# Optimization experiments

Hardware: AMD Instinct MI355X
Metric: run time of the kernel (lower is better)

Reference implementation:

```python
import jax, jax.numpy as jnp
import numpy as np

N_NODES = 100000
N_EDGES = 1600000
IN_C, HID_C, OUT_C = 128, 128, 64
BN_EPS = 1e-5


def _sage_conv(x, src, dst, w_self, w_neigh, b):
    # mean aggregation over incoming edges (gather -> segment-sum -> scale)
    deg = jax.ops.segment_sum(jnp.ones((src.shape[0],), x.dtype), dst, num_segments=N_NODES)
    agg = jax.ops.segment_sum(x[src], dst, num_segments=N_NODES)
    agg = agg / jnp.maximum(deg, 1.0)[:, None]
    return x @ w_self + agg @ w_neigh + b


def _batch_norm(x, gamma, beta):
    mean = x.mean(axis=0)
    var = x.var(axis=0)
    return (x - mean) * jax.lax.rsqrt(var + BN_EPS) * gamma + beta


def setup_inputs() -> dict:
    key = jax.random.key(0)
    ks = jax.random.split(key, 16)
    x = jax.random.normal(ks[0], (N_NODES, IN_C), dtype=jnp.float32)
    edge_index = jax.random.randint(ks[1], (2, N_EDGES), 0, N_NODES, dtype=jnp.int64)
    s = 0.05
    return {
        "x": x,
        "edge_index": edge_index,
        "w0_self": jax.random.normal(ks[2], (IN_C, HID_C), jnp.float32) * s,
        "w0_neigh": jax.random.normal(ks[3], (IN_C, HID_C), jnp.float32) * s,
        "b0": jnp.zeros((HID_C,), jnp.float32),
        "g0": jnp.ones((HID_C,), jnp.float32),
        "be0": jnp.zeros((HID_C,), jnp.float32),
        "w1_self": jax.random.normal(ks[4], (HID_C, HID_C), jnp.float32) * s,
        "w1_neigh": jax.random.normal(ks[5], (HID_C, HID_C), jnp.float32) * s,
        "b1": jnp.zeros((HID_C,), jnp.float32),
        "g1": jnp.ones((HID_C,), jnp.float32),
        "be1": jnp.zeros((HID_C,), jnp.float32),
        "w2_self": jax.random.normal(ks[6], (HID_C, OUT_C), jnp.float32) * s,
        "w2_neigh": jax.random.normal(ks[7], (HID_C, OUT_C), jnp.float32) * s,
        "b2": jnp.zeros((OUT_C,), jnp.float32),
    }


def reference(x, edge_index, w0_self, w0_neigh, b0, g0, be0,
              w1_self, w1_neigh, b1, g1, be1, w2_self, w2_neigh, b2):
    src, dst = edge_index[0], edge_index[1]
    # layer 0: conv -> BN -> ReLU (dropout is identity in eval)
    h = _sage_conv(x, src, dst, w0_self, w0_neigh, b0)
    h = jax.nn.relu(_batch_norm(h, g0, be0))
    # layer 1
    h = _sage_conv(h, src, dst, w1_self, w1_neigh, b1)
    h = jax.nn.relu(_batch_norm(h, g1, be1))
    # final conv + log_softmax
    h = _sage_conv(h, src, dst, w2_self, w2_neigh, b2)
    return jax.nn.log_softmax(h, axis=-1)
```

## Files before the change

kernel.cpp:

```cpp
#include <hip/hip_runtime.h>

typedef unsigned int uint;
typedef __attribute__((ext_vector_type(8))) short short8;
typedef __attribute__((ext_vector_type(4))) float f32x4;

#define N_NODES 100000
#define N_EDGES 1600000
#define NB_SCAN 391
#define CONVG_N 1563
#define EB 6250
#define TFG 12500

__device__ __forceinline__ float bflo(uint v) { return __uint_as_float(v << 16); }
__device__ __forceinline__ float bfhi(uint v) { return __uint_as_float(v & 0xffff0000u); }
__device__ __forceinline__ uint packbf2(float a, float b) {
    uint ua = __float_as_uint(a), ub = __float_as_uint(b);
    ua += 0x7fffu + ((ua >> 16) & 1u);
    ub += 0x7fffu + ((ub >> 16) & 1u);
    return (ua >> 16) | (ub & 0xffff0000u);
}

__device__ __forceinline__ void pack_w_body(const float* __restrict__ Wself,
                                            const float* __restrict__ Wneigh,
                                            uint* __restrict__ Wb, int OUTC, int NT, int i) {
    if (i >= 8 * NT * 64 * 4) return;
    int u = i & 3;
    int l = (i >> 2) & 63;
    int t = i >> 8;
    int c = t % NT, s = t / NT;
    int k = s * 32 + (l >> 4) * 8 + u * 2;
    int col = c * 16 + (l & 15);
    const float* W0 = (k < 128) ? (Wself + (size_t)k * OUTC)
                                : (Wneigh + (size_t)(k - 128) * OUTC);
    const float* W1 = (k + 1 < 128) ? (Wself + (size_t)(k + 1) * OUTC)
                                    : (Wneigh + (size_t)(k + 1 - 128) * OUTC);
    Wb[i] = packbf2(W0[col], W1[col]);
}

__global__ void prep_fused(const int* __restrict__ dst,
                           int* __restrict__ deg, int* __restrict__ rank,
                           const float* __restrict__ x, uint* __restrict__ ht2,
                           const float* __restrict__ w0s, const float* __restrict__ w0n, uint* __restrict__ wb0,
                           const float* __restrict__ w1s, const float* __restrict__ w1n, uint* __restrict__ wb1,
                           const float* __restrict__ w2s, const float* __restrict__ w2n, uint* __restrict__ wb2) {
    int b = blockIdx.x;
    int tid = threadIdx.x;
    if (b < EB) {
        int e = b * 256 + tid;
        if (e < N_EDGES) rank[e] = atomicAdd(&deg[dst[e]], 1);
    } else if (b < EB + TFG) {
        int i = (b - EB) * 256 + tid;
        if (i < N_NODES * 32) {
            int row = i >> 5, q = i & 31;
            float4 v = *(const float4*)(x + (size_t)row * 128 + q * 4);
            uint2 o;
            o.x = packbf2(v.x, v.y);
            o.y = packbf2(v.z, v.w);
            *(uint2*)(ht2 + (size_t)row * 64 + q * 2) = o;
        }
    } else if (b < EB + TFG + 64) {
        pack_w_body(w0s, w0n, wb0, 128, 8, (b - EB - TFG) * 256 + tid);
    } else if (b < EB + TFG + 128) {
        pack_w_body(w1s, w1n, wb1, 128, 8, (b - EB - TFG - 64) * 256 + tid);
    } else {
        pack_w_body(w2s, w2n, wb2, 64, 4, (b - EB - TFG - 128) * 256 + tid);
    }
}

__global__ void scan_blocksum(const int* __restrict__ deg, int* __restrict__ blk) {
    __shared__ int s[256];
    int i = blockIdx.x * 256 + threadIdx.x;
    s[threadIdx.x] = (i < N_NODES) ? deg[i] : 0;
    __syncthreads();
    for (int off = 128; off > 0; off >>= 1) {
        if (threadIdx.x < off) s[threadIdx.x] += s[threadIdx.x + off];
        __syncthreads();
    }
    if (threadIdx.x == 0) blk[blockIdx.x] = s[0];
}

__global__ void scan_blockoff(int* __restrict__ blk, int* __restrict__ row_ptr_last) {
    __shared__ int s[512];
    int t = threadIdx.x;
    int v = (t < NB_SCAN) ? blk[t] : 0;
    s[t] = v;
    __syncthreads();
    for (int off = 1; off < 512; off <<= 1) {
        int xv = (t >= off) ? s[t - off] : 0;
        __syncthreads();
        s[t] += xv;
        __syncthreads();
    }
    if (t < NB_SCAN) blk[t] = s[t] - v;
    if (t == NB_SCAN - 1) *row_ptr_last = s[t];
}

__global__ void scan_final(const int* __restrict__ deg, const int* __restrict__ blk,
                           int* __restrict__ row_ptr, float* __restrict__ invd) {
    __shared__ int s[256];
    int i = blockIdx.x * 256 + threadIdx.x;
    int v = (i < N_NODES) ? deg[i] : 0;
    s[threadIdx.x] = v;
    __syncthreads();
    for (int off = 1; off < 256; off <<= 1) {
        int xv = (threadIdx.x >= off) ? s[threadIdx.x - off] : 0;
        __syncthreads();
        s[threadIdx.x] += xv;
        __syncthreads();
    }
    if (i < N_NODES) {
        row_ptr[i] = blk[blockIdx.x] + s[threadIdx.x] - v;
        invd[i] = 1.0f / fmaxf((float)v, 1.0f);
    }
}

__global__ void fill_csr2(const int* __restrict__ src, const int* __restrict__ dst,
                          const int* __restrict__ row_ptr, const int* __restrict__ rank,
                          int* __restrict__ colx) {
    int e = blockIdx.x * blockDim.x + threadIdx.x;
    if (e < N_EDGES) colx[row_ptr[dst[e]] + rank[e]] = src[e];
}

template <bool TF>
__global__ void aggregate_bf16(const uint* __restrict__ H2,
                               const float* __restrict__ scale, const float* __restrict__ shift,
                               const int* __restrict__ row_ptr, const int* __restrict__ colx,
                               const float* __restrict__ invd, uint* __restrict__ agg2) {
    int lane = threadIdx.x & 63;
    int node = blockIdx.x * 4 + (threadIdx.x >> 6);
    if (node >= N_NODES) return;
    int beg = row_ptr[node], end = row_ptr[node + 1];
    float sc0 = 0.f, sc1 = 0.f, sh0 = 0.f, sh1 = 0.f;
    if (TF) {
        sc0 = scale[2 * lane];     sc1 = scale[2 * lane + 1];
        sh0 = shift[2 * lane];     sh1 = shift[2 * lane + 1];
    }
    float a0 = 0.f, a1 = 0.f;
    int j = beg;
#define ACC1(v)                                                        \
    if (TF) {                                                          \
        a0 += fmaxf(bflo(v) * sc0 + sh0, 0.f);                         \
        a1 += fmaxf(bfhi(v) * sc1 + sh1, 0.f);                         \
    } else {                                                           \
        a0 += bflo(v);                                                 \
        a1 += bfhi(v);                                                 \
    }
    for (; j + 8 <= end; j += 8) {
        int s0 = colx[j],     s1 = colx[j + 1], s2 = colx[j + 2], s3 = colx[j + 3];
        int s4 = colx[j + 4], s5 = colx[j + 5], s6 = colx[j + 6], s7 = colx[j + 7];
        uint v0 = H2[(size_t)s0 * 64 + lane];
        uint v1 = H2[(size_t)s1 * 64 + lane];
        uint v2 = H2[(size_t)s2 * 64 + lane];
        uint v3 = H2[(size_t)s3 * 64 + lane];
        uint v4 = H2[(size_t)s4 * 64 + lane];
        uint v5 = H2[(size_t)s5 * 64 + lane];
        uint v6 = H2[(size_t)s6 * 64 + lane];
        uint v7 = H2[(size_t)s7 * 64 + lane];
        ACC1(v0) ACC1(v1) ACC1(v2) ACC1(v3) ACC1(v4) ACC1(v5) ACC1(v6) ACC1(v7)
    }
    for (; j + 4 <= end; j += 4) {
        int s0 = colx[j], s1 = colx[j + 1], s2 = colx[j + 2], s3 = colx[j + 3];
        uint v0 = H2[(size_t)s0 * 64 + lane];
        uint v1 = H2[(size_t)s1 * 64 + lane];
        uint v2 = H2[(size_t)s2 * 64 + lane];
        uint v3 = H2[(size_t)s3 * 64 + lane];
        ACC1(v0) ACC1(v1) ACC1(v2) ACC1(v3)
    }
    for (; j < end; ++j) {
        uint v = H2[(size_t)colx[j] * 64 + lane];
        ACC1(v)
    }
#undef ACC1
    float id = invd[node];
    agg2[(size_t)node * 64 + lane] = packbf2(a0 * id, a1 * id);
}

template <int OUTC, bool STATS, bool BF16OUT, bool TF, bool LSM>
__global__ __launch_bounds__(256) void conv_mfma(
    const uint* __restrict__ Aself2, const uint* __restrict__ Agg2,
    const uint* __restrict__ Wb, const float* __restrict__ bias,
    const float* __restrict__ scale, const float* __restrict__ shift,
    float* __restrict__ OutF, uint* __restrict__ OutB, float* __restrict__ Ppart) {
    constexpr int NT = OUTC / 16;
    __shared__ float red[4][2 * OUTC];
    const int lane = threadIdx.x & 63;
    const int wv   = threadIdx.x >> 6;
    const int row0 = blockIdx.x * 64 + wv * 16;
    const int arow = row0 + (lane & 15);
    const bool aok = arow < N_NODES;
    const int kq   = lane >> 4;

    f32x4 acc[NT];
#pragma unroll
    for (int c = 0; c < NT; ++c) acc[c] = (f32x4){0.f, 0.f, 0.f, 0.f};

    union U { uint4 u; short8 s; };

#pragma unroll
    for (int s = 0; s < 8; ++s) {
        const uint* Asrc = (s < 4) ? Aself2 : Agg2;
        U a;
        a.u = make_uint4(0u, 0u, 0u, 0u);
        if (aok) {
            a.u = *(const uint4*)(Asrc + (size_t)arow * 64 + (s & 3) * 16 + kq * 4);
            if (TF && s < 4) {
                const int cb = (s & 3) * 32 + kq * 8;
                float4 sa = *(const float4*)(scale + cb);
                float4 sb = *(const float4*)(scale + cb + 4);
                float4 ha = *(const float4*)(shift + cb);
                float4 hb = *(const float4*)(shift + cb + 4);
                a.u.x = packbf2(fmaxf(bflo(a.u.x) * sa.x + ha.x, 0.f),
                                fmaxf(bfhi(a.u.x) * sa.y + ha.y, 0.f));
                a.u.y = packbf2(fmaxf(bflo(a.u.y) * sa.z + ha.z, 0.f),
                                fmaxf(bfhi(a.u.y) * sa.w + ha.w, 0.f));
                a.u.z = packbf2(fmaxf(bflo(a.u.z) * sb.x + hb.x, 0.f),
                                fmaxf(bfhi(a.u.z) * sb.y + hb.y, 0.f));
                a.u.w = packbf2(fmaxf(bflo(a.u.w) * sb.z + hb.z, 0.f),
                                fmaxf(bfhi(a.u.w) * sb.w + hb.w, 0.f));
            }
        }
#pragma unroll
        for (int c = 0; c < NT; ++c) {
            U b;
            b.u = *(const uint4*)(Wb + ((size_t)(s * NT + c) * 64 + lane) * 4);
            acc[c] = __builtin_amdgcn_mfma_f32_16x16x32_bf16(a.s, b.s, acc[c], 0, 0, 0);
        }
    }

    const int colbase = lane & 15;

    if (LSM) {
        float vb[NT][4];
#pragma unroll
        for (int c = 0; c < NT; ++c) {
            float bv = bias[c * 16 + colbase];
#pragma unroll
            for (int r = 0; r < 4; ++r) vb[c][r] = acc[c][r] + bv;
        }
#pragma unroll
        for (int r = 0; r < 4; ++r) {
            float m = fmaxf(fmaxf(vb[0][r], vb[1][r]), fmaxf(vb[2][r], vb[3][r]));
#pragma unroll
            for (int o = 8; o >= 1; o >>= 1) m = fmaxf(m, __shfl_xor(m, o));
            float ssum = (expf(vb[0][r] - m) + expf(vb[1][r] - m))
                       + (expf(vb[2][r] - m) + expf(vb[3][r] - m));
#pragma unroll
            for (int o = 8; o >= 1; o >>= 1) ssum += __shfl_xor(ssum, o);
            float lg = m + logf(ssum);
            int orow = row0 + kq * 4 + r;
            if (orow < N_NODES) {
#pragma unroll
                for (int c = 0; c < NT; ++c)
                    OutF[(size_t)orow * OUTC + c * 16 + colbase] = vb[c][r] - lg;
            }
        }
        return;
    }

#pragma unroll
    for (int c = 0; c < NT; ++c) {
        const int col = c * 16 + colbase;
        const float bv = bias[col];
        float sc = 0.f, qc = 0.f;
#pragma unroll
        for (int r = 0; r < 4; ++r) {
            int orow = row0 + kq * 4 + r;
            float v = acc[c][r] + bv;
            if (BF16OUT) {
                float vo = __shfl_xor(v, 1);
                if (orow < N_NODES) {
                    if ((colbase & 1) == 0)
                        OutB[(size_t)orow * (OUTC / 2) + (col >> 1)] = packbf2(v, vo);
                    if (STATS) { sc += v; qc += v * v; }
                }
            } else {
                if (orow < N_NODES) {
                    OutF[(size_t)orow * OUTC + col] = v;
                    if (STATS) { sc += v; qc += v * v; }
                }
            }
        }
        if (STATS) {
            sc += __shfl_xor(sc, 16); sc += __shfl_xor(sc, 32);
            qc += __shfl_xor(qc, 16); qc += __shfl_xor(qc, 32);
            if (kq == 0) {
                red[wv][col]        = sc;
                red[wv][OUTC + col] = qc;
            }
        }
    }
    if (STATS) {
        __syncthreads();
        int t = threadIdx.x;
        if (t < 2 * OUTC) {
            float p = red[0][t] + red[1][t] + red[2][t] + red[3][t];
            Ppart[(size_t)blockIdx.x * (2 * OUTC) + t] = p;
        }
    }
}

__global__ void bn_reduce32(const float* __restrict__ Ppart, float* __restrict__ pstage) {
    int t = threadIdx.x;
    float s = 0.f;
    for (int r = blockIdx.x; r < CONVG_N; r += 32)
        s += Ppart[(size_t)r * 256 + t];
    pstage[(size_t)blockIdx.x * 256 + t] = s;
}

__global__ void bn_finalize32(const float* __restrict__ pstage,
                              const float* __restrict__ g, const float* __restrict__ be,
                              float* __restrict__ scale, float* __restrict__ shift) {
    int c = threadIdx.x;
    float s = 0.f, q = 0.f;
    for (int r = 0; r < 32; ++r) {
        s += pstage[(size_t)r * 256 + c];
        q += pstage[(size_t)r * 256 + 128 + c];
    }
    float mean = s * (1.0f / N_NODES);
    float var  = q * (1.0f / N_NODES) - mean * mean;
    float inv  = rsqrtf(var + 1e-5f);
    float sc   = g[c] * inv;
    scale[c] = sc;
    shift[c] = be[c] - mean * sc;
}


extern "C" void kernel_launch(void* const* d_in, const int* in_sizes, int n_in,
                              void* d_out, int out_size, void* d_ws, size_t ws_size,
                              hipStream_t stream) {
    const float* x   = (const float*)d_in[0];
    const int*   ei  = (const int*)d_in[1];
    const float* w0s = (const float*)d_in[2];
    const float* w0n = (const float*)d_in[3];
    const float* b0  = (const float*)d_in[4];
    const float* g0  = (const float*)d_in[5];
    const float* be0 = (const float*)d_in[6];
    const float* w1s = (const float*)d_in[7];
    const float* w1n = (const float*)d_in[8];
    const float* b1  = (const float*)d_in[9];
    const float* g1  = (const float*)d_in[10];
    const float* be1 = (const float*)d_in[11];
    const float* w2s = (const float*)d_in[12];
    const float* w2n = (const float*)d_in[13];
    const float* b2  = (const float*)d_in[14];
    float* out = (float*)d_out;

    const int* src = ei;
    const int* dst = ei + N_EDGES;

    char* w = (char*)d_ws;
    size_t off = 0;
    auto alloc = [&](size_t bytes) {
        void* p = w + off;
        off += (bytes + 255) & ~(size_t)255;
        return p;
    };
    int*   deg     = (int*)alloc(N_NODES * 4);
    int*   row_ptr = (int*)alloc((N_NODES + 1) * 4);
    int*   blk     = (int*)alloc(512 * 4);
    int*   colx    = (int*)alloc((size_t)N_EDGES * 4);
    float* invd    = (float*)alloc(N_NODES * 4);
    float* pstage  = (float*)alloc(32 * 256 * 4);
    float* scale0  = (float*)alloc(128 * 4);
    float* shift0  = (float*)alloc(128 * 4);
    float* scale1  = (float*)alloc(128 * 4);
    float* shift1  = (float*)alloc(128 * 4);
    uint*  wb0     = (uint*)alloc(16384 * 4);
    uint*  wb1     = (uint*)alloc(16384 * 4);
    uint*  wb2     = (uint*)alloc(8192 * 4);
    float* ppart   = (float*)alloc((size_t)CONVG_N * 256 * 4);
    uint*  ht2     = (uint*)alloc((size_t)N_NODES * 64 * 4);
    uint*  agg2    = (uint*)alloc((size_t)N_NODES * 64 * 4);
    uint*  h2      = (uint*)alloc((size_t)N_NODES * 64 * 4);
    int*   rank    = (int*)agg2;

    const int NBk   = NB_SCAN;
    const int CONVG = CONVG_N;
    const int AGGG  = (N_NODES + 3) / 4;
    const int PREPG = EB + TFG + 128 + 32;

    hipMemsetAsync(deg, 0, N_NODES * 4, stream);
    prep_fused<<<PREPG, 256, 0, stream>>>(dst, deg, rank, x, ht2,
                                          w0s, w0n, wb0, w1s, w1n, wb1, w2s, w2n, wb2);
    scan_blocksum<<<NBk, 256, 0, stream>>>(deg, blk);
    scan_blockoff<<<1, 512, 0, stream>>>(blk, row_ptr + N_NODES);
    scan_final<<<NBk, 256, 0, stream>>>(deg, blk, row_ptr, invd);
    fill_csr2<<<EB, 256, 0, stream>>>(src, dst, row_ptr, rank, colx);

    aggregate_bf16<false><<<AGGG, 256, 0, stream>>>(ht2, nullptr, nullptr, row_ptr, colx, invd, agg2);
    conv_mfma<128, true, true, false, false><<<CONVG, 256, 0, stream>>>(
        ht2, agg2, wb0, b0, nullptr, nullptr, nullptr, h2, ppart);
    bn_reduce32<<<32, 256, 0, stream>>>(ppart, pstage);
    bn_finalize32<<<1, 128, 0, stream>>>(pstage, g0, be0, scale0, shift0);

    aggregate_bf16<true><<<AGGG, 256, 0, stream>>>(h2, scale0, shift0, row_ptr, colx, invd, agg2);
    conv_mfma<128, true, true, true, false><<<CONVG, 256, 0, stream>>>(
        h2, agg2, wb1, b1, scale0, shift0, nullptr, h2, ppart);
    bn_reduce32<<<32, 256, 0, stream>>>(ppart, pstage);
    bn_finalize32<<<1, 128, 0, stream>>>(pstage, g1, be1, scale1, shift1);

    aggregate_bf16<true><<<AGGG, 256, 0, stream>>>(h2, scale1, shift1, row_ptr, colx, invd, agg2);
    conv_mfma<64, false, false, true, true><<<CONVG, 256, 0, stream>>>(
        h2, agg2, wb2, b2, scale1, shift1, out, nullptr, nullptr);
}
```

Measured before the change: 426.0 us.

## Fuse neighbor mean aggregation into MFMA conv kernel via LDS staging

Each conv block now gathers and averages neighbor features for its 64 rows into shared memory, then feeds them directly to the MFMA loop. This removes the separate aggregate kernel and the global write and read of the aggregated tensor per layer. It uses ping-pong output buffers, since other blocks still read the input features. The cost is less gather parallelism: each wave processes 16 nodes sequentially instead of one node per wave.

```diff
diff --git a/kernel.cpp b/kernel.cpp
--- a/kernel.cpp
+++ b/kernel.cpp
@@ -121,72 +121,76 @@
     if (e < N_EDGES) colx[row_ptr[dst[e]] + rank[e]] = src[e];
 }
 
-template <bool TF>
-__global__ void aggregate_bf16(const uint* __restrict__ H2,
-                               const float* __restrict__ scale, const float* __restrict__ shift,
-                               const int* __restrict__ row_ptr, const int* __restrict__ colx,
-                               const float* __restrict__ invd, uint* __restrict__ agg2) {
-    int lane = threadIdx.x & 63;
-    int node = blockIdx.x * 4 + (threadIdx.x >> 6);
-    if (node >= N_NODES) return;
-    int beg = row_ptr[node], end = row_ptr[node + 1];
-    float sc0 = 0.f, sc1 = 0.f, sh0 = 0.f, sh1 = 0.f;
-    if (TF) {
-        sc0 = scale[2 * lane];     sc1 = scale[2 * lane + 1];
-        sh0 = shift[2 * lane];     sh1 = shift[2 * lane + 1];
-    }
-    float a0 = 0.f, a1 = 0.f;
-    int j = beg;
-#define ACC1(v)                                                        \
-    if (TF) {                                                          \
-        a0 += fmaxf(bflo(v) * sc0 + sh0, 0.f);                         \
-        a1 += fmaxf(bfhi(v) * sc1 + sh1, 0.f);                         \
-    } else {                                                           \
-        a0 += bflo(v);                                                 \
-        a1 += bfhi(v);                                                 \
-    }
-    for (; j + 8 <= end; j += 8) {
-        int s0 = colx[j],     s1 = colx[j + 1], s2 = colx[j + 2], s3 = colx[j + 3];
-        int s4 = colx[j + 4], s5 = colx[j + 5], s6 = colx[j + 6], s7 = colx[j + 7];
-        uint v0 = H2[(size_t)s0 * 64 + lane];
-        uint v1 = H2[(size_t)s1 * 64 + lane];
-        uint v2 = H2[(size_t)s2 * 64 + lane];
-        uint v3 = H2[(size_t)s3 * 64 + lane];
-        uint v4 = H2[(size_t)s4 * 64 + lane];
-        uint v5 = H2[(size_t)s5 * 64 + lane];
-        uint v6 = H2[(size_t)s6 * 64 + lane];
-        uint v7 = H2[(size_t)s7 * 64 + lane];
-        ACC1(v0) ACC1(v1) ACC1(v2) ACC1(v3) ACC1(v4) ACC1(v5) ACC1(v6) ACC1(v7)
-    }
-    for (; j + 4 <= end; j += 4) {
-        int s0 = colx[j], s1 = colx[j + 1], s2 = colx[j + 2], s3 = colx[j + 3];
-        uint v0 = H2[(size_t)s0 * 64 + lane];
-        uint v1 = H2[(size_t)s1 * 64 + lane];
-        uint v2 = H2[(size_t)s2 * 64 + lane];
-        uint v3 = H2[(size_t)s3 * 64 + lane];
-        ACC1(v0) ACC1(v1) ACC1(v2) ACC1(v3)
-    }
-    for (; j < end; ++j) {
-        uint v = H2[(size_t)colx[j] * 64 + lane];
-        ACC1(v)
-    }
-#undef ACC1
-    float id = invd[node];
-    agg2[(size_t)node * 64 + lane] = packbf2(a0 * id, a1 * id);
-}
-
 template <int OUTC, bool STATS, bool BF16OUT, bool TF, bool LSM>
-__global__ __launch_bounds__(256) void conv_mfma(
-    const uint* __restrict__ Aself2, const uint* __restrict__ Agg2,
+__global__ __launch_bounds__(256) void aggconv(
+    const uint* __restrict__ H2,
+    const float* __restrict__ scale, const float* __restrict__ shift,
+    const int* __restrict__ row_ptr, const int* __restrict__ colx,
+    const float* __restrict__ invd,
     const uint* __restrict__ Wb, const float* __restrict__ bias,
-    const float* __restrict__ scale, const float* __restrict__ shift,
     float* __restrict__ OutF, uint* __restrict__ OutB, float* __restrict__ Ppart) {
     constexpr int NT = OUTC / 16;
+    __shared__ uint aggL[64][68];
     __shared__ float red[4][2 * OUTC];
     const int lane = threadIdx.x & 63;
     const int wv   = threadIdx.x >> 6;
-    const int row0 = blockIdx.x * 64 + wv * 16;
-    const int arow = row0 + (lane & 15);
+    const int wrow0 = blockIdx.x * 64 + wv * 16;
+
+    {
+        float sc0 = 0.f, sc1 = 0.f, sh0 = 0.f, sh1 = 0.f;
+        if (TF) {
+            sc0 = scale[2 * lane];     sc1 = scale[2 * lane + 1];
+            sh0 = shift[2 * lane];     sh1 = shift[2 * lane + 1];
+        }
+#define ACC1(v)                                                        \
+        if (TF) {                                                      \
+            a0 += fmaxf(bflo(v) * sc0 + sh0, 0.f);                     \
+            a1 += fmaxf(bfhi(v) * sc1 + sh1, 0.f);                     \
+        } else {                                                       \
+            a0 += bflo(v);                                             \
+            a1 += bfhi(v);                                             \
+        }
+        for (int i = 0; i < 16; ++i) {
+            int node = wrow0 + i;
+            float a0 = 0.f, a1 = 0.f;
+            if (node < N_NODES) {
+                int beg = row_ptr[node], end = row_ptr[node + 1];
+                int j = beg;
+                for (; j + 8 <= end; j += 8) {
+                    int s0 = colx[j],     s1 = colx[j + 1], s2 = colx[j + 2], s3 = colx[j + 3];
+                    int s4 = colx[j + 4], s5 = colx[j + 5], s6 = colx[j + 6], s7 = colx[j + 7];
+                    uint v0 = H2[(size_t)s0 * 64 + lane];
+                    uint v1 = H2[(size_t)s1 * 64 + lane];
+                    uint v2 = H2[(size_t)s2 * 64 + lane];
+                    uint v3 = H2[(size_t)s3 * 64 + lane];
+                    uint v4 = H2[(size_t)s4 * 64 + lane];
+                    uint v5 = H2[(size_t)s5 * 64 + lane];
+                    uint v6 = H2[(size_t)s6 * 64 + lane];
+                    uint v7 = H2[(size_t)s7 * 64 + lane];
+                    ACC1(v0) ACC1(v1) ACC1(v2) ACC1(v3) ACC1(v4) ACC1(v5) ACC1(v6) ACC1(v7)
+                }
+                for (; j + 4 <= end; j += 4) {
+                    int s0 = colx[j], s1 = colx[j + 1], s2 = colx[j + 2], s3 = colx[j + 3];
+                    uint v0 = H2[(size_t)s0 * 64 + lane];
+                    uint v1 = H2[(size_t)s1 * 64 + lane];
+                    uint v2 = H2[(size_t)s2 * 64 + lane];
+                    uint v3 = H2[(size_t)s3 * 64 + lane];
+                    ACC1(v0) ACC1(v1) ACC1(v2) ACC1(v3)
+                }
+                for (; j < end; ++j) {
+                    uint v = H2[(size_t)colx[j] * 64 + lane];
+                    ACC1(v)
+                }
+                float id = invd[node];
+                a0 *= id; a1 *= id;
+            }
+            aggL[wv * 16 + i][lane] = packbf2(a0, a1);
+        }
+#undef ACC1
+    }
+    __syncthreads();
+
+    const int arow = wrow0 + (lane & 15);
     const bool aok = arow < N_NODES;
     const int kq   = lane >> 4;
 
@@ -198,26 +202,29 @@
 
 #pragma unroll
     for (int s = 0; s < 8; ++s) {
-        const uint* Asrc = (s < 4) ? Aself2 : Agg2;
         U a;
-        a.u = make_uint4(0u, 0u, 0u, 0u);
-        if (aok) {
-            a.u = *(const uint4*)(Asrc + (size_t)arow * 64 + (s & 3) * 16 + kq * 4);
-            if (TF && s < 4) {
-                const int cb = (s & 3) * 32 + kq * 8;
-                float4 sa = *(const float4*)(scale + cb);
-                float4 sb = *(const float4*)(scale + cb + 4);
-                float4 ha = *(const float4*)(shift + cb);
-                float4 hb = *(const float4*)(shift + cb + 4);
-                a.u.x = packbf2(fmaxf(bflo(a.u.x) * sa.x + ha.x, 0.f),
-                                fmaxf(bfhi(a.u.x) * sa.y + ha.y, 0.f));
-                a.u.y = packbf2(fmaxf(bflo(a.u.y) * sa.z + ha.z, 0.f),
-                                fmaxf(bfhi(a.u.y) * sa.w + ha.w, 0.f));
-                a.u.z = packbf2(fmaxf(bflo(a.u.z) * sb.x + hb.x, 0.f),
-                                fmaxf(bfhi(a.u.z) * sb.y + hb.y, 0.f));
-                a.u.w = packbf2(fmaxf(bflo(a.u.w) * sb.z + hb.z, 0.f),
-                                fmaxf(bfhi(a.u.w) * sb.w + hb.w, 0.f));
+        if (s < 4) {
+            a.u = make_uint4(0u, 0u, 0u, 0u);
+            if (aok) {
+                a.u = *(const uint4*)(H2 + (size_t)arow * 64 + (s & 3) * 16 + kq * 4);
+                if (TF) {
+                    const int cb = (s & 3) * 32 + kq * 8;
+                    float4 sa = *(const float4*)(scale + cb);
+                    float4 sb = *(const float4*)(scale + cb + 4);
+                    float4 ha = *(const float4*)(shift + cb);
+                    float4 hb = *(const float4*)(shift + cb + 4);
+                    a.u.x = packbf2(fmaxf(bflo(a.u.x) * sa.x + ha.x, 0.f),
+                                    fmaxf(bfhi(a.u.x) * sa.y + ha.y, 0.f));
+                    a.u.y = packbf2(fmaxf(bflo(a.u.y) * sa.z + ha.z, 0.f),
+                                    fmaxf(bfhi(a.u.y) * sa.w + ha.w, 0.f));
+                    a.u.z = packbf2(fmaxf(bflo(a.u.z) * sb.x + hb.x, 0.f),
+                                    fmaxf(bfhi(a.u.z) * sb.y + hb.y, 0.f));
+                    a.u.w = packbf2(fmaxf(bflo(a.u.w) * sb.z + hb.z, 0.f),
+                                    fmaxf(bfhi(a.u.w) * sb.w + hb.w, 0.f));
+                }
             }
+        } else {
+            a.u = *(const uint4*)&aggL[wv * 16 + (lane & 15)][(s & 3) * 16 + kq * 4];
         }
 #pragma unroll
         for (int c = 0; c < NT; ++c) {
@@ -247,7 +254,7 @@
 #pragma unroll
             for (int o = 8; o >= 1; o >>= 1) ssum += __shfl_xor(ssum, o);
             float lg = m + logf(ssum);
-            int orow = row0 + kq * 4 + r;
+            int orow = wrow0 + kq * 4 + r;
             if (orow < N_NODES) {
 #pragma unroll
                 for (int c = 0; c < NT; ++c)
@@ -264,7 +271,7 @@
         float sc = 0.f, qc = 0.f;
 #pragma unroll
         for (int r = 0; r < 4; ++r) {
-            int orow = row0 + kq * 4 + r;
+            int orow = wrow0 + kq * 4 + r;
             float v = acc[c][r] + bv;
             if (BF16OUT) {
                 float vo = __shfl_xor(v, 1);
@@ -370,13 +377,12 @@
     uint*  wb2     = (uint*)alloc(8192 * 4);
     float* ppart   = (float*)alloc((size_t)CONVG_N * 256 * 4);
     uint*  ht2     = (uint*)alloc((size_t)N_NODES * 64 * 4);
-    uint*  agg2    = (uint*)alloc((size_t)N_NODES * 64 * 4);
-    uint*  h2      = (uint*)alloc((size_t)N_NODES * 64 * 4);
-    int*   rank    = (int*)agg2;
+    uint*  h2a     = (uint*)alloc((size_t)N_NODES * 64 * 4);
+    uint*  h2b     = (uint*)alloc((size_t)N_NODES * 64 * 4);
+    int*   rank    = (int*)h2a;
 
     const int NBk   = NB_SCAN;
     const int CONVG = CONVG_N;
-    const int AGGG  = (N_NODES + 3) / 4;
     const int PREPG = EB + TFG + 128 + 32;
 
     hipMemsetAsync(deg, 0, N_NODES * 4, stream);
@@ -387,19 +393,16 @@
     scan_final<<<NBk, 256, 0, stream>>>(deg, blk, row_ptr, invd);
     fill_csr2<<<EB, 256, 0, stream>>>(src, dst, row_ptr, rank, colx);
 
-    aggregate_bf16<false><<<AGGG, 256, 0, stream>>>(ht2, nullptr, nullptr, row_ptr, colx, invd, agg2);
-    conv_mfma<128, true, true, false, false><<<CONVG, 256, 0, stream>>>(
-        ht2, agg2, wb0, b0, nullptr, nullptr, nullptr, h2, ppart);
+    aggconv<128, true, true, false, false><<<CONVG, 256, 0, stream>>>(
+        ht2, nullptr, nullptr, row_ptr, colx, invd, wb0, b0, nullptr, h2a, ppart);
     bn_reduce32<<<32, 256, 0, stream>>>(ppart, pstage);
     bn_finalize32<<<1, 128, 0, stream>>>(pstage, g0, be0, scale0, shift0);
 
-    aggregate_bf16<true><<<AGGG, 256, 0, stream>>>(h2, scale0, shift0, row_ptr, colx, invd, agg2);
-    conv_mfma<128, true, true, true, false><<<CONVG, 256, 0, stream>>>(
-        h2, agg2, wb1, b1, scale0, shift0, nullptr, h2, ppart);
+    aggconv<128, true, true, true, false><<<CONVG, 256, 0, stream>>>(
+        h2a, scale0, shift0, row_ptr, colx, invd, wb1, b1, nullptr, h2b, ppart);
     bn_reduce32<<<32, 256, 0, stream>>>(ppart, pstage);
     bn_finalize32<<<1, 128, 0, stream>>>(pstage, g1, be1, scale1, shift1);
 
-    aggregate_bf16<true><<<AGGG, 256, 0, stream>>>(h2, scale1, shift1, row_ptr, colx, invd, agg2);
-    conv_mfma<64, false, false, true, true><<<CONVG, 256, 0, stream>>>(
-        h2, agg2, wb2, b2, scale1, shift1, out, nullptr, nullptr);
-}
+    aggconv<64, false, false, true, true><<<CONVG, 256, 0, stream>>>(
+        h2b, scale1, shift1, row_ptr, colx, invd, wb2, b2, out, nullptr, nullptr);
+}
```

Result: slower. 488.4 us (+14.6%).
